# Kernel optimization log

Measured on AMD Instinct MI355X. Metric: run time of the kernel, lower is better.

The kernel has to match this reference:

```python
import jax, jax.numpy as jnp
import numpy as np

N = 200_000; E = 800_000; NS = 400_000; ES = 1_600_000
B = 512; PPG = 8; PT = 4
NF = 64; NE = 16; H = 128; RW = 16; PRW = 16; L = 4


def _scatter_mean(v, idx, num_segments):
    s = jax.ops.segment_sum(v, idx, num_segments=num_segments)
    c = jax.ops.segment_sum(jnp.ones((v.shape[0], 1), v.dtype), idx, num_segments=num_segments)
    return s / jnp.maximum(c, 1.0)


def _mpnn(h, edge_index, edge_attr, edge_weight, We, be, Wl, bl):
    # WDNodeMPNN: edge-feature encoder + L rounds of weighted gather/scatter message passing.
    src, dst = edge_index[0], edge_index[1]
    e = jax.nn.relu(edge_attr @ We + be)                      # [E, H]
    n = h.shape[0]
    for l in range(Wl.shape[0]):
        msg = (h[src] + e) * edge_weight[:, None]             # gather + weight
        agg = jax.ops.segment_sum(msg, dst, num_segments=n)   # scatter-add
        h = jax.nn.relu(jnp.concatenate([h, agg], axis=-1) @ Wl[l] + bl[l])
    return h


def _bn(v, g, b, eps=1e-5):
    m = v.mean(0)
    var = v.var(0)
    return (v - m) * jax.lax.rsqrt(var + eps) * g + b


def setup_inputs() -> dict:
    key = jax.random.key(0)
    ks = jax.random.split(key, 48)
    f = lambda i, shape, s=1.0: jax.random.normal(ks[i], shape, dtype=jnp.float32) * s
    inp = {
        'x': f(0, (N, NF)),
        'rw_pos_enc': f(1, (N, RW)),
        'node_weight': jax.random.uniform(ks[2], (N,), dtype=jnp.float32),
        'edge_index': jax.random.randint(ks[3], (2, E), 0, N),
        'edge_attr': f(4, (E, NE)),
        'edge_weight': jax.random.uniform(ks[5], (E,), dtype=jnp.float32),
        'patch_pe': f(6, (B * PPG, PRW)),
        'subgraphs_nodes_mapper': jax.random.randint(ks[7], (NS,), 0, N),
        'combined_subgraphs': jax.random.randint(ks[8], (2, ES), 0, NS),
        'subgraphs_edges_mapper': jax.random.randint(ks[9], (ES,), 0, E),
        'subgraphs_batch': jnp.sort(jax.random.randint(ks[10], (NS,), 0, B * PPG)),
        'context_subgraph_idx': jax.random.randint(ks[11], (B,), 0, PPG),
        'target_subgraph_idxs': jax.random.randint(ks[12], (B, PT), 0, PPG),
        'patches_per_graph': PPG,
        'W_in': f(13, (NF, H), NF ** -0.5), 'b_in': jnp.zeros((H,), jnp.float32),
        'W_rw': f(14, (RW, H), RW ** -0.5), 'b_rw': jnp.zeros((H,), jnp.float32),
        'W_prw': f(15, (PRW, H), PRW ** -0.5), 'b_prw': jnp.zeros((H,), jnp.float32),
        'ctx_We': f(16, (NE, H), NE ** -0.5), 'ctx_be': jnp.zeros((H,), jnp.float32),
        'ctx_Wl': f(17, (L, 2 * H, H), (2 * H) ** -0.5), 'ctx_bl': jnp.zeros((L, H), jnp.float32),
        'tgt_We': f(18, (NE, H), NE ** -0.5), 'tgt_be': jnp.zeros((H,), jnp.float32),
        'tgt_Wl': f(19, (L, 2 * H, H), (2 * H) ** -0.5), 'tgt_bl': jnp.zeros((L, H), jnp.float32),
        'Wp1': f(20, (H, H), H ** -0.5), 'bp1': jnp.zeros((H,), jnp.float32),
        'g1': jnp.ones((H,), jnp.float32), 'be1': jnp.zeros((H,), jnp.float32),
        'Wp2': f(21, (H, H), H ** -0.5), 'bp2': jnp.zeros((H,), jnp.float32),
        'g2': jnp.ones((H,), jnp.float32), 'be2': jnp.zeros((H,), jnp.float32),
        'Wp3': f(22, (H, H), H ** -0.5), 'bp3': jnp.zeros((H,), jnp.float32),
    }
    return inp


def reference(x, rw_pos_enc, node_weight, edge_index, edge_attr, edge_weight, patch_pe,
              subgraphs_nodes_mapper, combined_subgraphs, subgraphs_edges_mapper,
              subgraphs_batch, context_subgraph_idx, target_subgraph_idxs, patches_per_graph,
              W_in, b_in, W_rw, b_rw, W_prw, b_prw,
              ctx_We, ctx_be, ctx_Wl, ctx_bl, tgt_We, tgt_be, tgt_Wl, tgt_bl,
              Wp1, bp1, g1, be1, Wp2, bp2, g2, be2, Wp3, bp3):
    n_graphs = context_subgraph_idx.shape[0]
    n_patches = n_graphs * patches_per_graph
    nhid = W_in.shape[1]

    # shared node embedding: input_encoder(x) + rw_encoder(rw_pos_enc)
    x0 = (x @ W_in + b_in) + (rw_pos_enc @ W_rw + b_rw)        # [N, H]

    # --- context branch on batched subgraphs ---
    xs = x0[subgraphs_nodes_mapper]                             # [Ns, H]
    ea_s = edge_attr[subgraphs_edges_mapper]                    # [Es, NE]
    ew_s = edge_weight[subgraphs_edges_mapper]                  # [Es]
    hs = _mpnn(xs, combined_subgraphs, ea_s, ew_s, ctx_We, ctx_be, ctx_Wl, ctx_bl)
    emb_sub = _scatter_mean(hs, subgraphs_batch, n_patches)     # [P, H]

    batch_indexer = jnp.arange(n_graphs, dtype=context_subgraph_idx.dtype) * patches_per_graph
    ctx_idx = context_subgraph_idx + batch_indexer
    emb_ctx = emb_sub[ctx_idx]                                  # [B, H]

    # --- target branch on full graph (no_grad in the original) ---
    full_h = jax.lax.stop_gradient(
        _mpnn(x0, edge_index, edge_attr, edge_weight, tgt_We, tgt_be, tgt_Wl, tgt_bl))
    sub_from_full = _scatter_mean(full_h[subgraphs_nodes_mapper], subgraphs_batch, n_patches)

    tidx = (target_subgraph_idxs + batch_indexer[:, None]).reshape(-1)   # [B*PT]
    emb_tgt = sub_from_full[tidx].reshape(n_graphs, -1, nhid)            # [B, PT, H]

    # PE-conditioned prediction of target patches from context embedding
    enc_pes = patch_pe[tidx] @ W_prw + b_prw                              # [B*PT, H]
    cond = (emb_ctx[:, None, :] + enc_pes.reshape(n_graphs, -1, nhid)).reshape(-1, nhid)
    p = jax.nn.relu(_bn(cond @ Wp1 + bp1, g1, be1))
    p = jax.nn.relu(_bn(p @ Wp2 + bp2, g2, be2))
    pred = (p @ Wp3 + bp3).reshape(n_graphs, -1, nhid)                    # [B, PT, H]

    return jnp.stack([emb_tgt, pred])                                     # [2, B, PT, H]
```

## Files before the change

kernel.cpp:

```cpp
#include <hip/hip_runtime.h>

#define HH 128
constexpr int cN   = 200000;
constexpr int cE   = 800000;
constexpr int cNS  = 400000;
constexpr int cES  = 1600000;
constexpr int cB   = 512;
constexpr int cPPG = 8;
constexpr int cPT  = 4;
constexpr int cNP  = cB * cPPG;
constexpr int cNF  = 64;
constexpr int cNE  = 16;
constexpr int cRW  = 16;
constexpr int cPRW = 16;
constexpr int cL   = 4;

typedef __attribute__((ext_vector_type(8))) short s16x8;
typedef __attribute__((ext_vector_type(4))) float f32x4;

__device__ __forceinline__ float b2f(unsigned short b) {
    return __uint_as_float(((unsigned int)b) << 16);
}
__device__ __forceinline__ unsigned short f2b(float f) {
    unsigned int u = __float_as_uint(f);
    return (unsigned short)((u + 0x7fffu + ((u >> 16) & 1u)) >> 16);
}

__global__ void k_diag(float* __restrict__ out, int n, float val) {
    int gid = blockIdx.x * 256 + threadIdx.x;
    if (gid < n) out[gid] = val;
}

__global__ void k_zero_int(int* __restrict__ p, int n) {
    int i = blockIdx.x * 256 + threadIdx.x;
    if (i < n) p[i] = 0;
}
__global__ void k_copy_int(const int* __restrict__ a, int* __restrict__ b, int n) {
    int i = blockIdx.x * 256 + threadIdx.x;
    if (i < n) b[i] = a[i];
}

__global__ void k_ea16(const float* __restrict__ eattr, unsigned short* __restrict__ ea16, int n) {
    int i = blockIdx.x * 256 + threadIdx.x;
    if (i < n) ea16[i] = f2b(eattr[i]);
}

__global__ void k_hist(const int* __restrict__ dst, int* __restrict__ cnt, int ne) {
    int e = blockIdx.x * 256 + threadIdx.x;
    if (e < ne) atomicAdd(&cnt[dst[e]], 1);
}

__global__ void k_scan_local(const int* __restrict__ cnt, int* __restrict__ rp1,
                             int* __restrict__ bsum, int n) {
    __shared__ int s[256];
    int t = threadIdx.x;
    int i = blockIdx.x * 256 + t;
    s[t] = (i < n) ? cnt[i] : 0;
    __syncthreads();
    for (int off = 1; off < 256; off <<= 1) {
        int u = (t >= off) ? s[t - off] : 0;
        __syncthreads();
        s[t] += u;
        __syncthreads();
    }
    if (i < n) rp1[i] = s[t];
    if (t == 255) bsum[blockIdx.x] = s[255];
}

__global__ void k_scan_bsums(int* __restrict__ bsum, int nb) {
    __shared__ int s[256];
    __shared__ int carry;
    int t = threadIdx.x;
    if (t == 0) carry = 0;
    __syncthreads();
    for (int base = 0; base < nb; base += 256) {
        int i = base + t;
        s[t] = (i < nb) ? bsum[i] : 0;
        __syncthreads();
        for (int off = 1; off < 256; off <<= 1) {
            int u = (t >= off) ? s[t - off] : 0;
            __syncthreads();
            s[t] += u;
            __syncthreads();
        }
        int c = carry;
        if (i < nb) bsum[i] = s[t] + c;
        __syncthreads();
        if (t == 0) carry = c + s[255];
        __syncthreads();
    }
}

__global__ void k_rp_finalize(const int* __restrict__ bsum, int* __restrict__ rp, int n) {
    int i = blockIdx.x * 256 + threadIdx.x;
    if (i == 0) rp[0] = 0;
    if (i < n) {
        int blk = i >> 8;
        rp[i + 1] += blk ? bsum[blk - 1] : 0;
    }
}

__global__ void k_scatter(const int* __restrict__ src, const int* __restrict__ dst,
                          const int* __restrict__ emap, int* __restrict__ cursor,
                          int* __restrict__ srcs, int* __restrict__ ais, int ne) {
    int e = blockIdx.x * 256 + threadIdx.x;
    if (e >= ne) return;
    int d = dst[e];
    int p = atomicAdd(&cursor[d], 1);
    srcs[p] = src[e];
    ais[p] = emap ? emap[e] : e;
}

__global__ void k_wfrag_all(const float* __restrict__ cWl, const float* __restrict__ tWl,
                            const float* __restrict__ cWe, const float* __restrict__ tWe,
                            unsigned short* __restrict__ fC, unsigned short* __restrict__ fTH,
                            unsigned short* __restrict__ fTL,
                            unsigned short* __restrict__ wezC,
                            unsigned short* __restrict__ wezTH,
                            unsigned short* __restrict__ wezTL) {
    int g = blockIdx.x * 256 + threadIdx.x;
    int set = g >> 12;
    int r = g & 4095;
    if (set == 12) {
        if (r < 1536) {
            int sub = r >> 9;
            int rr = r & 511;
            int ct = rr >> 6, lane = rr & 63;
            const float* We = (sub == 0) ? cWe : tWe;
            unsigned short* o = (sub == 0) ? wezC : (sub == 1 ? wezTH : wezTL);
#pragma unroll
            for (int j = 0; j < 8; j++) {
                int k = (lane >> 4) * 8 + j;
                unsigned short v = 0;
                if (k < 16) {
                    float w = We[k * HH + ct * 16 + (lane & 15)];
                    unsigned short hi = f2b(w);
                    v = (sub == 2) ? f2b(w - b2f(hi)) : hi;
                }
                o[((size_t)ct * 64 + lane) * 8 + j] = v;
            }
        }
        return;
    }
    int ct = r >> 9, ks = (r >> 6) & 7, lane = r & 63;
    const float* W;
    unsigned short* outp;
    bool lo = false;
    if (set < 4)      { W = cWl + (size_t)set * 2 * HH * HH;       outp = fC  + (size_t)set * 32768; }
    else if (set < 8) { W = tWl + (size_t)(set - 4) * 2 * HH * HH; outp = fTH + (size_t)(set - 4) * 32768; }
    else              { W = tWl + (size_t)(set - 8) * 2 * HH * HH; outp = fTL + (size_t)(set - 8) * 32768; lo = true; }
#pragma unroll
    for (int j = 0; j < 8; j++) {
        float w = W[(size_t)(ks * 32 + (lane >> 4) * 8 + j) * HH + ct * 16 + (lane & 15)];
        unsigned short hi = f2b(w);
        outp[(size_t)r * 8 + j] = lo ? f2b(w - b2f(hi)) : hi;
    }
}

template <bool BF16OUT>
__global__ void __launch_bounds__(256)
k_encode16(const float* __restrict__ x, const float* __restrict__ rw,
           const int* __restrict__ map,
           const float* __restrict__ Win, const float* __restrict__ bin,
           const float* __restrict__ Wrw, const float* __restrict__ brw,
           void* __restrict__ outv) {
    __shared__ float sx[16][cNF];
    __shared__ float srw[16][cRW];
    int t = threadIdx.x;
    int nb = blockIdx.x * 16;
    {
        int n = t >> 4, v = t & 15;
        int node = map ? map[nb + n] : (nb + n);
        ((float4*)&sx[n][0])[v] = ((const float4*)&x[(size_t)node * cNF])[v];
        if (v < 4) ((float4*)&srw[n][0])[v] = ((const float4*)&rw[(size_t)node * cRW])[v];
    }
    int c = t & 127;
    float wcol[cNF], wrcol[cRW];
#pragma unroll
    for (int k = 0; k < cNF; k++) wcol[k] = Win[k * HH + c];
#pragma unroll
    for (int k = 0; k < cRW; k++) wrcol[k] = Wrw[k * HH + c];
    float bsum = bin[c] + brw[c];
    __syncthreads();

#pragma unroll
    for (int p = 0; p < 8; p++) {
        int n = (p * 256 + t) >> 7;
        float acc = bsum;
#pragma unroll
        for (int k = 0; k < cNF; k += 4) {
            float4 s4 = *(const float4*)&sx[n][k];
            acc += s4.x * wcol[k] + s4.y * wcol[k + 1] + s4.z * wcol[k + 2] + s4.w * wcol[k + 3];
        }
#pragma unroll
        for (int k = 0; k < cRW; k += 4) {
            float4 s4 = *(const float4*)&srw[n][k];
            acc += s4.x * wrcol[k] + s4.y * wrcol[k + 1] + s4.z * wrcol[k + 2] + s4.w * wrcol[k + 3];
        }
        size_t oidx = (size_t)(nb + n) * HH + c;
        if (BF16OUT) ((unsigned short*)outv)[oidx] = f2b(acc);
        else         ((float*)outv)[oidx] = acc;
    }
}

__global__ void __launch_bounds__(256)
k_layer_ctx(const unsigned short* __restrict__ h_in, unsigned short* __restrict__ h_out,
            const int* __restrict__ rp, const int* __restrict__ srcs,
            const int* __restrict__ ais, const unsigned short* __restrict__ ea16,
            const float* __restrict__ ew,
            const unsigned short* __restrict__ wez, const float* __restrict__ be,
            const unsigned short* __restrict__ Wfrag, const float* __restrict__ bias) {
    __shared__ unsigned short pool[8704];
    __shared__ float wsl[64];
    auto msg = (unsigned short (*)[136])pool;
    auto At  = (unsigned short (*)[264])pool;
    int t = threadIdx.x;
    int base = blockIdx.x * 32;
    int lane = t & 63, wv = t >> 6, ar = lane & 15, g4 = lane >> 4;

    s16x8 bez[2];
    float beq[2];
#pragma unroll
    for (int q = 0; q < 2; q++) {
        bez[q] = *(const s16x8*)&wez[((size_t)(2 * wv + q) * 64 + lane) * 8];
        beq[q] = be[(2 * wv + q) * 16 + ar];
    }
    int eblk0 = rp[base], eblk1 = rp[base + 32];
    int prow = t >> 3, pch = (t & 7) * 16;
    int re0 = rp[base + prow], re1 = rp[base + prow + 1];
    float acc[16];
#pragma unroll
    for (int j = 0; j < 16; j++) acc[j] = 0.f;

    for (int cs = eblk0; cs < eblk1; cs += 64) {
        int ce = min(cs + 64, eblk1);
        if (t < 64) {
            int e = cs + t;
            if (e < ce) wsl[t] = ew[ais[e]];
        }
        {
            f32x4 cac[4][2];
#pragma unroll
            for (int rt = 0; rt < 4; rt++)
#pragma unroll
                for (int q = 0; q < 2; q++) cac[rt][q] = (f32x4)(0.f);
#pragma unroll
            for (int rt = 0; rt < 4; rt++) {
                s16x8 af = {0, 0, 0, 0, 0, 0, 0, 0};
                int row = cs + rt * 16 + ar;
                if (g4 < 2 && row < eblk1)
                    af = *(const s16x8*)&ea16[(size_t)ais[row] * cNE + g4 * 8];
#pragma unroll
                for (int q = 0; q < 2; q++)
                    cac[rt][q] = __builtin_amdgcn_mfma_f32_16x16x32_bf16(af, bez[q], cac[rt][q], 0, 0, 0);
            }
#pragma unroll
            for (int rt = 0; rt < 4; rt++)
#pragma unroll
                for (int q = 0; q < 2; q++) {
                    int col = (2 * wv + q) * 16 + ar;
#pragma unroll
                    for (int qi = 0; qi < 4; qi++)
                        msg[rt * 16 + g4 * 4 + qi][col] = f2b(fmaxf(cac[rt][q][qi] + beq[q], 0.f));
                }
        }
        __syncthreads();
        {
            int e0 = max(re0, cs), e1 = min(re1, ce);
            for (int e = e0; e < e1; e++) {
                int sl = e - cs;
                float w = wsl[sl];
                int s = srcs[e];
                const unsigned short* hrow = &h_in[(size_t)s * HH + pch];
                s16x8 hv0 = *(const s16x8*)&hrow[0];
                s16x8 hv1 = *(const s16x8*)&hrow[8];
                s16x8 mv0 = *(const s16x8*)&msg[sl][pch];
                s16x8 mv1 = *(const s16x8*)&msg[sl][pch + 8];
#pragma unroll
                for (int j = 0; j < 8; j++) {
                    acc[j]     += (b2f((unsigned short)hv0[j]) + b2f((unsigned short)mv0[j])) * w;
                    acc[8 + j] += (b2f((unsigned short)hv1[j]) + b2f((unsigned short)mv1[j])) * w;
                }
            }
        }
        __syncthreads();
    }
#pragma unroll
    for (int j = 0; j < 16; j++) At[prow][HH + pch + j] = f2b(acc[j]);
    for (int i = t; i < 512; i += 256) {
        int r = i >> 4, cc = (i & 15) * 8;
        *(s16x8*)&At[r][cc] = *(const s16x8*)&h_in[(size_t)(base + r) * HH + cc];
    }
    __syncthreads();

    f32x4 ac[2][2];
#pragma unroll
    for (int i1 = 0; i1 < 2; i1++)
#pragma unroll
        for (int i2 = 0; i2 < 2; i2++) ac[i1][i2] = (f32x4)(0.f);
#pragma unroll
    for (int ks = 0; ks < 8; ks++) {
        int ak = ks * 32 + g4 * 8;
        s16x8 a0 = *(const s16x8*)&At[ar][ak];
        s16x8 a1 = *(const s16x8*)&At[16 + ar][ak];
#pragma unroll
        for (int q = 0; q < 2; q++) {
            int ct = 2 * wv + q;
            s16x8 bq = *(const s16x8*)&Wfrag[((size_t)(ct * 8 + ks) * 64 + lane) * 8];
            ac[0][q] = __builtin_amdgcn_mfma_f32_16x16x32_bf16(a0, bq, ac[0][q], 0, 0, 0);
            ac[1][q] = __builtin_amdgcn_mfma_f32_16x16x32_bf16(a1, bq, ac[1][q], 0, 0, 0);
        }
    }
#pragma unroll
    for (int rt = 0; rt < 2; rt++)
#pragma unroll
        for (int q = 0; q < 2; q++) {
            int col = (2 * wv + q) * 16 + ar;
            float bv = bias[col];
#pragma unroll
            for (int qi = 0; qi < 4; qi++) {
                int row = base + rt * 16 + g4 * 4 + qi;
                h_out[(size_t)row * HH + col] = f2b(fmaxf(ac[rt][q][qi] + bv, 0.f));
            }
        }
}

__global__ void __launch_bounds__(256)
k_layer_tgt(const float* __restrict__ h_in, float* __restrict__ h_out,
            const int* __restrict__ rp, const int* __restrict__ srcs,
            const int* __restrict__ ais,
            const float* __restrict__ eattr, const float* __restrict__ ew,
            const unsigned short* __restrict__ wezH, const unsigned short* __restrict__ wezL,
            const float* __restrict__ be,
            const unsigned short* __restrict__ WfH, const unsigned short* __restrict__ WfL,
            const float* __restrict__ bias) {
    __shared__ unsigned short pool[16896];
    __shared__ float wsl[64];
    auto msg  = (float (*)[132])pool;
    auto AtH  = (unsigned short (*)[264])pool;
    auto AtL  = (unsigned short (*)[264])(pool + 8448);
    int t = threadIdx.x;
    int base = blockIdx.x * 32;
    int lane = t & 63, wv = t >> 6, ar = lane & 15, g4 = lane >> 4;

    s16x8 bezH[2], bezL[2];
    float beq[2];
#pragma unroll
    for (int q = 0; q < 2; q++) {
        bezH[q] = *(const s16x8*)&wezH[((size_t)(2 * wv + q) * 64 + lane) * 8];
        bezL[q] = *(const s16x8*)&wezL[((size_t)(2 * wv + q) * 64 + lane) * 8];
        beq[q] = be[(2 * wv + q) * 16 + ar];
    }
    int eblk0 = rp[base], eblk1 = rp[base + 32];
    int prow = t >> 3, pch = (t & 7) * 16;
    int re0 = rp[base + prow], re1 = rp[base + prow + 1];
    float acc[16];
#pragma unroll
    for (int j = 0; j < 16; j++) acc[j] = 0.f;

    for (int cs = eblk0; cs < eblk1; cs += 64) {
        int ce = min(cs + 64, eblk1);
        if (t < 64) {
            int e = cs + t;
            if (e < ce) wsl[t] = ew[ais[e]];
        }
        {
            f32x4 cac[4][2];
#pragma unroll
            for (int rt = 0; rt < 4; rt++)
#pragma unroll
                for (int q = 0; q < 2; q++) cac[rt][q] = (f32x4)(0.f);
#pragma unroll
            for (int rt = 0; rt < 4; rt++) {
                s16x8 afH = {0, 0, 0, 0, 0, 0, 0, 0};
                s16x8 afL = {0, 0, 0, 0, 0, 0, 0, 0};
                int row = cs + rt * 16 + ar;
                if (g4 < 2 && row < eblk1) {
                    const float* ea = eattr + (size_t)ais[row] * cNE + g4 * 8;
                    float4 lo4 = *(const float4*)ea;
                    float4 hi4 = *(const float4*)(ea + 4);
                    float vv[8];
                    *(float4*)&vv[0] = lo4;
                    *(float4*)&vv[4] = hi4;
#pragma unroll
                    for (int j = 0; j < 8; j++) {
                        unsigned short hi = f2b(vv[j]);
                        afH[j] = (short)hi;
                        afL[j] = (short)f2b(vv[j] - b2f(hi));
                    }
                }
#pragma unroll
                for (int q = 0; q < 2; q++) {
                    cac[rt][q] = __builtin_amdgcn_mfma_f32_16x16x32_bf16(afH, bezH[q], cac[rt][q], 0, 0, 0);
                    cac[rt][q] = __builtin_amdgcn_mfma_f32_16x16x32_bf16(afL, bezH[q], cac[rt][q], 0, 0, 0);
                    cac[rt][q] = __builtin_amdgcn_mfma_f32_16x16x32_bf16(afH, bezL[q], cac[rt][q], 0, 0, 0);
                }
            }
#pragma unroll
            for (int rt = 0; rt < 4; rt++)
#pragma unroll
                for (int q = 0; q < 2; q++) {
                    int col = (2 * wv + q) * 16 + ar;
#pragma unroll
                    for (int qi = 0; qi < 4; qi++)
                        msg[rt * 16 + g4 * 4 + qi][col] = fmaxf(cac[rt][q][qi] + beq[q], 0.f);
                }
        }
        __syncthreads();
        {
            int e0 = max(re0, cs), e1 = min(re1, ce);
            for (int e = e0; e < e1; e++) {
                int sl = e - cs;
                float w = wsl[sl];
                int s = srcs[e];
                const float* hrow = &h_in[(size_t)s * HH + pch];
#pragma unroll
                for (int j = 0; j < 16; j += 4) {
                    float4 hv = *(const float4*)&hrow[j];
                    float4 mv = *(const float4*)&msg[sl][pch + j];
                    acc[j]     += (hv.x + mv.x) * w;
                    acc[j + 1] += (hv.y + mv.y) * w;
                    acc[j + 2] += (hv.z + mv.z) * w;
                    acc[j + 3] += (hv.w + mv.w) * w;
                }
            }
        }
        __syncthreads();
    }
#pragma unroll
    for (int j = 0; j < 16; j++) {
        float v = acc[j];
        unsigned short hi = f2b(v);
        AtH[prow][HH + pch + j] = hi;
        AtL[prow][HH + pch + j] = f2b(v - b2f(hi));
    }
    for (int i = t; i < 32 * HH; i += 256) {
        int r = i >> 7, c = i & 127;
        float v = h_in[(size_t)(base + r) * HH + c];
        unsigned short hi = f2b(v);
        AtH[r][c] = hi;
        AtL[r][c] = f2b(v - b2f(hi));
    }
    __syncthreads();

    f32x4 ac[2][2];
#pragma unroll
    for (int i1 = 0; i1 < 2; i1++)
#pragma unroll
        for (int i2 = 0; i2 < 2; i2++) ac[i1][i2] = (f32x4)(0.f);
#pragma unroll
    for (int ks = 0; ks < 8; ks++) {
        int ak = ks * 32 + g4 * 8;
        s16x8 a0h = *(const s16x8*)&AtH[ar][ak];
        s16x8 a1h = *(const s16x8*)&AtH[16 + ar][ak];
        s16x8 a0l = *(const s16x8*)&AtL[ar][ak];
        s16x8 a1l = *(const s16x8*)&AtL[16 + ar][ak];
#pragma unroll
        for (int q = 0; q < 2; q++) {
            int ct = 2 * wv + q;
            size_t fo = ((size_t)(ct * 8 + ks) * 64 + lane) * 8;
            s16x8 bh = *(const s16x8*)&WfH[fo];
            s16x8 bl = *(const s16x8*)&WfL[fo];
            ac[0][q] = __builtin_amdgcn_mfma_f32_16x16x32_bf16(a0h, bh, ac[0][q], 0, 0, 0);
            ac[0][q] = __builtin_amdgcn_mfma_f32_16x16x32_bf16(a0l, bh, ac[0][q], 0, 0, 0);
            ac[0][q] = __builtin_amdgcn_mfma_f32_16x16x32_bf16(a0h, bl, ac[0][q], 0, 0, 0);
            ac[1][q] = __builtin_amdgcn_mfma_f32_16x16x32_bf16(a1h, bh, ac[1][q], 0, 0, 0);
            ac[1][q] = __builtin_amdgcn_mfma_f32_16x16x32_bf16(a1l, bh, ac[1][q], 0, 0, 0);
            ac[1][q] = __builtin_amdgcn_mfma_f32_16x16x32_bf16(a1h, bl, ac[1][q], 0, 0, 0);
        }
    }
#pragma unroll
    for (int rt = 0; rt < 2; rt++)
#pragma unroll
        for (int q = 0; q < 2; q++) {
            int col = (2 * wv + q) * 16 + ar;
            float bv = bias[col];
#pragma unroll
            for (int qi = 0; qi < 4; qi++) {
                int row = base + rt * 16 + g4 * 4 + qi;
                h_out[(size_t)row * HH + col] = fmaxf(ac[rt][q][qi] + bv, 0.f);
            }
        }
}

__global__ void k_seg_mean_f32(const float* __restrict__ src, const int* __restrict__ map,
                               const int* __restrict__ batch, float* __restrict__ out, int nrows) {
    int b = blockIdx.x;
    int t = threadIdx.x;
    int lo = 0, hi = nrows;
    while (lo < hi) { int m = (lo + hi) >> 1; if (batch[m] < b) lo = m + 1; else hi = m; }
    int s = lo;
    hi = nrows;
    while (lo < hi) { int m = (lo + hi) >> 1; if (batch[m] < b + 1) lo = m + 1; else hi = m; }
    int e = lo;
    float acc = 0.f;
    for (int r = s; r < e; r++) {
        size_t row = map ? (size_t)map[r] : (size_t)r;
        acc += src[row * HH + t];
    }
    out[(size_t)b * HH + t] = acc / fmaxf((float)(e - s), 1.f);
}

__global__ void k_seg_mean_bf16(const unsigned short* __restrict__ src,
                                const int* __restrict__ batch, float* __restrict__ out, int nrows) {
    int b = blockIdx.x;
    int t = threadIdx.x;
    int lo = 0, hi = nrows;
    while (lo < hi) { int m = (lo + hi) >> 1; if (batch[m] < b) lo = m + 1; else hi = m; }
    int s = lo;
    hi = nrows;
    while (lo < hi) { int m = (lo + hi) >> 1; if (batch[m] < b + 1) lo = m + 1; else hi = m; }
    int e = lo;
    float acc = 0.f;
    for (int r = s; r < e; r++) acc += b2f(src[(size_t)r * HH + t]);
    out[(size_t)b * HH + t] = acc / fmaxf((float)(e - s), 1.f);
}

__global__ void k_cond(const float* __restrict__ mctx, const float* __restrict__ mtgt,
                       const int* __restrict__ cidx, const int* __restrict__ tgt_idxs,
                       const float* __restrict__ ppe, const float* __restrict__ Wprw,
                       const float* __restrict__ bprw, float* __restrict__ cond,
                       float* __restrict__ out0) {
    int r = blockIdx.x;
    int t = threadIdx.x;
    int bg = r >> 2, tt = r & 3;
    int ti = tgt_idxs[bg * cPT + tt] + bg * cPPG;
    int ci = cidx[bg] + bg * cPPG;
    __shared__ float pe[cPRW];
    if (t < cPRW) pe[t] = ppe[(size_t)ti * cPRW + t];
    __syncthreads();
    float acc = bprw[t];
#pragma unroll
    for (int k = 0; k < cPRW; k++) acc += pe[k] * Wprw[k * HH + t];
    cond[(size_t)r * HH + t] = mctx[(size_t)ci * HH + t] + acc;
    out0[(size_t)r * HH + t] = mtgt[(size_t)ti * HH + t];
}

__global__ void k_gemm_h(const float* __restrict__ x, const float* __restrict__ W,
                         const float* __restrict__ b, float* __restrict__ y) {
    int r = blockIdx.x;
    int t = threadIdx.x;
    __shared__ float xr[HH];
    xr[t] = x[(size_t)r * HH + t];
    __syncthreads();
    float acc = b[t];
#pragma unroll 8
    for (int k = 0; k < HH; k++) acc += xr[k] * W[k * HH + t];
    y[(size_t)r * HH + t] = acc;
}

__global__ void k_bn_stats(const float* __restrict__ x, float* __restrict__ stats, int rows) {
    int c = blockIdx.x;
    int t = threadIdx.x;
    float s = 0.f, sq = 0.f;
    for (int r = t; r < rows; r += 256) {
        float v = x[(size_t)r * HH + c];
        s += v; sq += v * v;
    }
    __shared__ float bs[256], bq[256];
    bs[t] = s; bq[t] = sq;
    __syncthreads();
    for (int o = 128; o > 0; o >>= 1) {
        if (t < o) { bs[t] += bs[t + o]; bq[t] += bq[t + o]; }
        __syncthreads();
    }
    if (t == 0) {
        float m = bs[0] / rows;
        float var = bq[0] / rows - m * m;
        stats[c] = m;
        stats[HH + c] = rsqrtf(var + 1e-5f);
    }
}

__global__ void k_bn_relu(float* __restrict__ x, const float* __restrict__ stats,
                          const float* __restrict__ g, const float* __restrict__ be, int rows) {
    int gid = blockIdx.x * 256 + threadIdx.x;
    if (gid >= rows * HH) return;
    int c = gid & 127;
    float v = (x[gid] - stats[c]) * stats[HH + c] * g[c] + be[c];
    x[gid] = fmaxf(v, 0.f);
}

static void build_csr(const int* src, const int* dst, const int* emap, int nnodes, int ne,
                      int* rp, int* srcs, int* ais, int* cursor, int* bsum,
                      hipStream_t stream) {
    int nb = (nnodes + 255) / 256;
    k_zero_int<<<nb, 256, 0, stream>>>(cursor, nnodes);
    k_hist<<<(ne + 255) / 256, 256, 0, stream>>>(dst, cursor, ne);
    k_scan_local<<<nb, 256, 0, stream>>>(cursor, rp + 1, bsum, nnodes);
    k_scan_bsums<<<1, 256, 0, stream>>>(bsum, nb);
    k_rp_finalize<<<nb, 256, 0, stream>>>(bsum, rp, nnodes);
    k_copy_int<<<nb, 256, 0, stream>>>(rp, cursor, nnodes);
    k_scatter<<<(ne + 255) / 256, 256, 0, stream>>>(src, dst, emap, cursor, srcs, ais, ne);
}

extern "C" void kernel_launch(void* const* d_in, const int* in_sizes, int n_in,
                              void* d_out, int out_size, void* d_ws, size_t ws_size,
                              hipStream_t stream) {
    (void)in_sizes; (void)n_in;
    const float* x      = (const float*)d_in[0];
    const float* rw     = (const float*)d_in[1];
    const int*   eidx   = (const int*)d_in[3];
    const float* eattr  = (const float*)d_in[4];
    const float* ew     = (const float*)d_in[5];
    const float* ppe    = (const float*)d_in[6];
    const int*   nmap   = (const int*)d_in[7];
    const int*   csub   = (const int*)d_in[8];
    const int*   semap  = (const int*)d_in[9];
    const int*   sbatch = (const int*)d_in[10];
    const int*   cidx   = (const int*)d_in[11];
    const int*   tgts   = (const int*)d_in[12];
    const float* Win  = (const float*)d_in[14]; const float* bin  = (const float*)d_in[15];
    const float* Wrw  = (const float*)d_in[16]; const float* brw  = (const float*)d_in[17];
    const float* Wprw = (const float*)d_in[18]; const float* bprw = (const float*)d_in[19];
    const float* cWe  = (const float*)d_in[20]; const float* cbe  = (const float*)d_in[21];
    const float* cWl  = (const float*)d_in[22]; const float* cbl  = (const float*)d_in[23];
    const float* tWe  = (const float*)d_in[24]; const float* tbe  = (const float*)d_in[25];
    const float* tWl  = (const float*)d_in[26]; const float* tbl  = (const float*)d_in[27];
    const float* Wp1  = (const float*)d_in[28]; const float* bp1  = (const float*)d_in[29];
    const float* g1   = (const float*)d_in[30]; const float* be1  = (const float*)d_in[31];
    const float* Wp2  = (const float*)d_in[32]; const float* bp2  = (const float*)d_in[33];
    const float* g2   = (const float*)d_in[34]; const float* be2  = (const float*)d_in[35];
    const float* Wp3  = (const float*)d_in[36]; const float* bp3  = (const float*)d_in[37];
    float* out = (float*)d_out;

    const size_t R = (size_t)cN * HH * sizeof(float);
    char* base = (char*)d_ws;
    float* R0f = (float*)base;
    float* R1f = (float*)(base + R);
    unsigned short* R0h = (unsigned short*)base;
    unsigned short* R1h = (unsigned short*)(base + R);
    int* ip = (int*)(base + 2 * R);
    int* rp_t  = ip;  ip += cN + 1;
    int* rp_c  = ip;  ip += cNS + 1;
    int* src_t = ip;  ip += cE;
    int* ai_t  = ip;  ip += cE;
    int* src_c = ip;  ip += cES;
    int* ai_c  = ip;  ip += cES;
    int* cursor = ip; ip += cNS;
    int* bsum  = ip;  ip += 2048;
    char* cp = (char*)(((uintptr_t)ip + 15) & ~(uintptr_t)15);
    unsigned short* wfragC  = (unsigned short*)cp;
    unsigned short* wfragTH = wfragC + (size_t)4 * 32768;
    unsigned short* wfragTL = wfragTH + (size_t)4 * 32768;
    unsigned short* wez_c   = wfragTL + (size_t)4 * 32768;
    unsigned short* wez_tH  = wez_c + 4096;
    unsigned short* wez_tL  = wez_tH + 4096;
    unsigned short* ea16    = wez_tL + 4096;
    cp += ((size_t)12 * 32768 + 3 * 4096 + (size_t)cE * cNE) * sizeof(unsigned short);
    float* fp  = (float*)cp;
    float* mctx = fp; fp += (size_t)cNP * HH;
    float* mtgt = fp; fp += (size_t)cNP * HH;
    float* bufc = fp; fp += (size_t)2048 * HH;
    float* bufa = fp; fp += (size_t)2048 * HH;
    float* bufb = fp; fp += (size_t)2048 * HH;
    float* stats = fp; fp += 256;
    const size_t need = (size_t)((char*)fp - base);
    if (ws_size < need) {
        k_diag<<<(out_size + 255) / 256, 256, 0, stream>>>(out, out_size,
                                                           (float)(ws_size >> 20));
        return;
    }

    build_csr(eidx, eidx + cE, nullptr, cN, cE, rp_t, src_t, ai_t, cursor, bsum, stream);
    build_csr(csub, csub + cES, semap, cNS, cES, rp_c, src_c, ai_c, cursor, bsum, stream);
    k_wfrag_all<<<208, 256, 0, stream>>>(cWl, tWl, cWe, tWe, wfragC, wfragTH, wfragTL,
                                         wez_c, wez_tH, wez_tL);
    k_ea16<<<(cE * cNE + 255) / 256, 256, 0, stream>>>(eattr, ea16, cE * cNE);

    k_encode16<false><<<cN / 16, 256, 0, stream>>>(x, rw, nullptr, Win, bin, Wrw, brw, R0f);
    {
        float* hp[2] = { R0f, R1f };
        for (int l = 0; l < cL; l++) {
            k_layer_tgt<<<cN / 32, 256, 0, stream>>>(
                hp[l & 1], hp[(l & 1) ^ 1], rp_t, src_t, ai_t,
                eattr, ew, wez_tH, wez_tL, tbe,
                wfragTH + (size_t)l * 32768, wfragTL + (size_t)l * 32768, tbl + l * HH);
        }
    }
    k_seg_mean_f32<<<cNP, 128, 0, stream>>>(R0f, nmap, sbatch, mtgt, cNS);

    k_encode16<true><<<cNS / 16, 256, 0, stream>>>(x, rw, nmap, Win, bin, Wrw, brw, R0h);
    {
        unsigned short* hp[2] = { R0h, R1h };
        for (int l = 0; l < cL; l++) {
            k_layer_ctx<<<cNS / 32, 256, 0, stream>>>(
                hp[l & 1], hp[(l & 1) ^ 1], rp_c, src_c, ai_c, ea16,
                ew, wez_c, cbe, wfragC + (size_t)l * 32768, cbl + l * HH);
        }
    }
    k_seg_mean_bf16<<<cNP, 128, 0, stream>>>(R0h, sbatch, mctx, cNS);

    k_cond<<<cB * cPT, 128, 0, stream>>>(mctx, mtgt, cidx, tgts, ppe, Wprw, bprw, bufc, out);
    k_gemm_h<<<2048, 128, 0, stream>>>(bufc, Wp1, bp1, bufa);
    k_bn_stats<<<HH, 256, 0, stream>>>(bufa, stats, 2048);
    k_bn_relu<<<(2048 * HH) / 256, 256, 0, stream>>>(bufa, stats, g1, be1, 2048);
    k_gemm_h<<<2048, 128, 0, stream>>>(bufa, Wp2, bp2, bufb);
    k_bn_stats<<<HH, 256, 0, stream>>>(bufb, stats, 2048);
    k_bn_relu<<<(2048 * HH) / 256, 256, 0, stream>>>(bufb, stats, g2, be2, 2048);
    k_gemm_h<<<2048, 128, 0, stream>>>(bufb, Wp3, bp3, out + (size_t)2048 * HH);
}
```

Before: 3.022 ms.

## Make context-layer edge encoding per-wavefront to drop block-wide barriers

```diff
diff --git a/kernel.cpp b/kernel.cpp
--- a/kernel.cpp
+++ b/kernel.cpp
@@ -210,72 +210,64 @@
             const float* __restrict__ ew,
             const unsigned short* __restrict__ wez, const float* __restrict__ be,
             const unsigned short* __restrict__ Wfrag, const float* __restrict__ bias) {
-    __shared__ unsigned short pool[8704];
-    __shared__ float wsl[64];
-    auto msg = (unsigned short (*)[136])pool;
-    auto At  = (unsigned short (*)[264])pool;
+    __shared__ unsigned short pool[17408];
+    __shared__ float wslw[4][16];
+    auto At = (unsigned short (*)[264])pool;
     int t = threadIdx.x;
     int base = blockIdx.x * 32;
     int lane = t & 63, wv = t >> 6, ar = lane & 15, g4 = lane >> 4;
-
-    s16x8 bez[2];
-    float beq[2];
-#pragma unroll
-    for (int q = 0; q < 2; q++) {
-        bez[q] = *(const s16x8*)&wez[((size_t)(2 * wv + q) * 64 + lane) * 8];
-        beq[q] = be[(2 * wv + q) * 16 + ar];
-    }
-    int eblk0 = rp[base], eblk1 = rp[base + 32];
+    unsigned short (*msgw)[136] = (unsigned short (*)[136])(pool + (size_t)wv * 16 * 136);
+
+    s16x8 bez[8];
+    float beq[8];
+#pragma unroll
+    for (int q = 0; q < 8; q++) {
+        bez[q] = *(const s16x8*)&wez[((size_t)q * 64 + lane) * 8];
+        beq[q] = be[q * 16 + ar];
+    }
+
+    int we0 = rp[base + wv * 8], we1 = rp[base + wv * 8 + 8];
     int prow = t >> 3, pch = (t & 7) * 16;
     int re0 = rp[base + prow], re1 = rp[base + prow + 1];
     float acc[16];
 #pragma unroll
     for (int j = 0; j < 16; j++) acc[j] = 0.f;
 
-    for (int cs = eblk0; cs < eblk1; cs += 64) {
-        int ce = min(cs + 64, eblk1);
-        if (t < 64) {
-            int e = cs + t;
-            if (e < ce) wsl[t] = ew[ais[e]];
+    for (int cs = we0; cs < we1; cs += 16) {
+        int ce = min(cs + 16, we1);
+        if (lane < 16) {
+            int e = cs + lane;
+            if (e < ce) wslw[wv][lane] = ew[ais[e]];
         }
         {
-            f32x4 cac[4][2];
-#pragma unroll
-            for (int rt = 0; rt < 4; rt++)
-#pragma unroll
-                for (int q = 0; q < 2; q++) cac[rt][q] = (f32x4)(0.f);
-#pragma unroll
-            for (int rt = 0; rt < 4; rt++) {
-                s16x8 af = {0, 0, 0, 0, 0, 0, 0, 0};
-                int row = cs + rt * 16 + ar;
-                if (g4 < 2 && row < eblk1)
-                    af = *(const s16x8*)&ea16[(size_t)ais[row] * cNE + g4 * 8];
-#pragma unroll
-                for (int q = 0; q < 2; q++)
-                    cac[rt][q] = __builtin_amdgcn_mfma_f32_16x16x32_bf16(af, bez[q], cac[rt][q], 0, 0, 0);
-            }
-#pragma unroll
-            for (int rt = 0; rt < 4; rt++)
-#pragma unroll
-                for (int q = 0; q < 2; q++) {
-                    int col = (2 * wv + q) * 16 + ar;
-#pragma unroll
-                    for (int qi = 0; qi < 4; qi++)
-                        msg[rt * 16 + g4 * 4 + qi][col] = f2b(fmaxf(cac[rt][q][qi] + beq[q], 0.f));
-                }
-        }
-        __syncthreads();
+            s16x8 af = {0, 0, 0, 0, 0, 0, 0, 0};
+            int row = cs + ar;
+            if (g4 < 2 && row < ce)
+                af = *(const s16x8*)&ea16[(size_t)ais[row] * cNE + g4 * 8];
+            f32x4 cac[8];
+#pragma unroll
+            for (int q = 0; q < 8; q++) cac[q] = (f32x4)(0.f);
+#pragma unroll
+            for (int q = 0; q < 8; q++)
+                cac[q] = __builtin_amdgcn_mfma_f32_16x16x32_bf16(af, bez[q], cac[q], 0, 0, 0);
+#pragma unroll
+            for (int q = 0; q < 8; q++)
+#pragma unroll
+                for (int qi = 0; qi < 4; qi++)
+                    msgw[g4 * 4 + qi][q * 16 + ar] = f2b(fmaxf(cac[q][qi] + beq[q], 0.f));
+        }
+        asm volatile("" ::: "memory");
         {
             int e0 = max(re0, cs), e1 = min(re1, ce);
             for (int e = e0; e < e1; e++) {
                 int sl = e - cs;
-                float w = wsl[sl];
+                float w = wslw[wv][sl];
                 int s = srcs[e];
                 const unsigned short* hrow = &h_in[(size_t)s * HH + pch];
                 s16x8 hv0 = *(const s16x8*)&hrow[0];
                 s16x8 hv1 = *(const s16x8*)&hrow[8];
-                s16x8 mv0 = *(const s16x8*)&msg[sl][pch];
-                s16x8 mv1 = *(const s16x8*)&msg[sl][pch + 8];
+                s16x8 mv0 = *(const s16x8*)&msgw[sl][pch];
+                s16x8 mv1 = *(const s16x8*)&msgw[sl][pch + 8];
 #pragma unroll
                 for (int j = 0; j < 8; j++) {
                     acc[j]     += (b2f((unsigned short)hv0[j]) + b2f((unsigned short)mv0[j])) * w;
@@ -283,8 +275,9 @@
                 }
             }
         }
-        __syncthreads();
-    }
+        asm volatile("" ::: "memory");
+    }
+    __syncthreads();
 #pragma unroll
     for (int j = 0; j < 16; j++) At[prow][HH + pch + j] = f2b(acc[j]);
     for (int i = t; i < 512; i += 256) {
```

After: 3.237 ms. 7.1% more time.
